# Kernel optimization log

Hardware: AMD Instinct MI355X
Metric: run time of the kernel (lower is better)

Reference implementation:

```python
import jax, jax.numpy as jnp
import numpy as np

B, N, D_IN, D_EMB = 8, 2048, 768, 768

def setup_inputs() -> dict:
    key = jax.random.key(0)
    k1, k2, k3, k4 = jax.random.split(key, 4)
    x = jax.random.normal(k1, (B, N, D_IN), dtype=jnp.float32)
    # nn.Linear weights stored as [out, in]; applied as x @ W.T
    Wq = jax.random.normal(k2, (D_EMB, D_IN), dtype=jnp.float32) * (D_IN ** -0.5)
    Wk = jax.random.normal(k3, (D_EMB, D_IN), dtype=jnp.float32) * (D_IN ** -0.5)
    Wv = jax.random.normal(k4, (D_EMB, D_IN), dtype=jnp.float32) * (D_IN ** -0.5)
    return {"x": x, "Wq": Wq, "Wk": Wk, "Wv": Wv}

def reference(x, Wq, Wk, Wv):
    dim_sqrt = jnp.asarray(D_EMB ** 0.5, x.dtype)
    q = jnp.einsum('bnd,ed->bne', x, Wq)  # [B,N,E]
    k = jnp.einsum('bnd,ed->bne', x, Wk)
    v = jnp.einsum('bnd,ed->bne', x, Wv)
    scores = jnp.einsum('bne,bme->bnm', q, k)  # [B,N,N]
    # NOTE: module applies softmax FIRST, then divides by sqrt(d) (post-hoc)
    attn = jax.nn.softmax(scores, axis=-1) / dim_sqrt
    out = jnp.einsum('bnm,bme->bne', attn, v)
    return out
```

## Files before the change

kernel.cpp:

```cpp
#include <hip/hip_runtime.h>
#include <stdint.h>
#include <type_traits>

typedef __bf16 bf16;
typedef _Float16 f16;
typedef bf16 bf16x8 __attribute__((ext_vector_type(8)));
typedef f16 f16x8 __attribute__((ext_vector_type(8)));
typedef float f32x4 __attribute__((ext_vector_type(4)));

#define LOG2E 1.4426950408889634f
#define SQRT_E 27.712812921102035f

enum { EPI_F32 = 0, EPI_PAIR = 1, EPI_VT = 2, EPI_F16 = 3 };

__device__ __forceinline__ void async16(const void* g, void* l) {
  __builtin_amdgcn_global_load_lds(
      (__attribute__((address_space(1))) void*)(uintptr_t)g,
      (__attribute__((address_space(3))) void*)l, 16, 0, 0);
}

__device__ __forceinline__ f32x4 mfma8(bf16x8 a, bf16x8 b, f32x4 c) {
  return __builtin_amdgcn_mfma_f32_16x16x32_bf16(a, b, c, 0, 0, 0);
}
__device__ __forceinline__ f32x4 mfma8(f16x8 a, f16x8 b, f32x4 c) {
  return __builtin_amdgcn_mfma_f32_16x16x32_f16(a, b, c, 0, 0, 0);
}

template <int N>
__device__ __forceinline__ void vwait() {
  asm volatile("s_waitcnt vmcnt(%0)" ::"i"(N) : "memory");
}
__device__ __forceinline__ void block_bar() {
  asm volatile("" ::: "memory");
  __builtin_amdgcn_s_barrier();
  asm volatile("" ::: "memory");
}

template <typename T, typename TO, int BMt, int BNt, int BKt, int AT, int EPI>
__global__ __launch_bounds__((BMt == 256 ? 512 : 256), 2)
void gemm_pipe(const T* __restrict__ Ah, const T* __restrict__ Al,
               const T* __restrict__ Bh, void* __restrict__ C0,
               int K, long lda, long ldb, long ldc,
               long stA, long stB, long stC, int gxN, int gyM) {
  using vec8 = typename std::conditional<std::is_same<T, bf16>::value,
                                         bf16x8, f16x8>::type;
  static_assert(BMt == BNt, "square tiles only");
  constexpr int THREADS = (BMt == 256) ? 512 : 256;
  constexpr int NWN = (BMt == 256) ? 4 : 2;
  constexpr int WTM = BMt / 2;
  constexpr int WTN = BNt / NWN;
  static_assert(WTN == 64, "wave tile must be 64 wide");
  constexpr int MF = WTM / 16;
  constexpr int KK = BKt / 32;
  constexpr int CPR = BKt / 8;
  constexpr int RPI = THREADS / CPR;
  constexpr int LPP = (BMt * BKt) / (THREADS * 8);
  constexpr int LPT = LPP * (AT == 2 ? 3 : 2);

  __shared__ __align__(16) T sA[2][BMt * BKt];
  __shared__ __align__(16) T sB[2][BNt * BKt];
  __shared__ __align__(16) T sAl[AT == 2 ? 2 * BMt * BKt : 8];

  const int id = blockIdx.x;
  const int xcd = id & 7;
  const int j0 = id >> 3;
  const int s = j0 / gxN;
  const int bxi = j0 - s * gxN;
  const int g = xcd + 8 * s;
  const int byi = g % gyM;
  const int z = g / gyM;

  const T* pA = Ah + (long)z * stA;
  const T* pB = Bh + (long)z * stB;
  const T* pAl = (AT == 2) ? Al : nullptr;

  const int bm = byi * BMt;
  const int bn = bxi * BNt;
  const int tid = threadIdx.x;
  const int wave = tid >> 6;
  const int lane = tid & 63;
  const int wm = (wave / NWN) * WTM;
  const int wn = (wave % NWN) * WTN;
  const int quad = lane >> 4;
  const int l16 = lane & 15;

  f32x4 acc[MF][4] = {};

  const int srow = tid / CPR;
  const int schk = tid % CPR;
  const int swc = ((BKt == 64) ? (schk ^ (srow & 7)) : schk) * 8;
  const int cs0 = (quad * 8) ^ ((BKt == 64) ? ((l16 & 7) << 3) : 0);

  const int NT = K / BKt;

  auto stage = [&](int buf, int t) {
    const long ka = (long)t * BKt + swc;
#pragma unroll
    for (int l = 0; l < LPP; ++l)
      async16(pA + (long)(bm + l * RPI + srow) * lda + ka,
              &sA[buf][(l * THREADS + tid) * 8]);
#pragma unroll
    for (int l = 0; l < LPP; ++l)
      async16(pB + (long)(bn + l * RPI + srow) * ldb + ka,
              &sB[buf][(l * THREADS + tid) * 8]);
    if constexpr (AT == 2) {
#pragma unroll
      for (int l = 0; l < LPP; ++l)
        async16(pAl + (long)(bm + l * RPI + srow) * lda + ka,
                &sAl[buf * BMt * BKt + (l * THREADS + tid) * 8]);
    }
  };

  auto compute = [&](int buf) {
    const T* bA = &sA[buf][0];
    const T* bB = &sB[buf][0];
    const T* bAl = (AT == 2) ? &sAl[buf * BMt * BKt] : nullptr;
    vec8 bf[KK][4];
#pragma unroll
    for (int kk = 0; kk < KK; ++kk)
#pragma unroll
      for (int jj = 0; jj < 4; ++jj)
        bf[kk][jj] =
            *(const vec8*)&bB[(wn + jj * 16 + l16) * BKt + (cs0 ^ (kk * 32))];
#pragma unroll
    for (int mq = 0; mq < MF / 2; ++mq) {
      vec8 af[KK][2];
      vec8 alf[AT == 2 ? KK : 1][2];
#pragma unroll
      for (int kk = 0; kk < KK; ++kk)
#pragma unroll
        for (int ii = 0; ii < 2; ++ii) {
          const int r = wm + mq * 32 + ii * 16 + l16;
          af[kk][ii] = *(const vec8*)&bA[r * BKt + (cs0 ^ (kk * 32))];
          if constexpr (AT == 2)
            alf[kk][ii] = *(const vec8*)&bAl[r * BKt + (cs0 ^ (kk * 32))];
        }
      __builtin_amdgcn_s_setprio(1);
#pragma unroll
      for (int jj = 0; jj < 4; ++jj)
#pragma unroll
        for (int ii = 0; ii < 2; ++ii)
#pragma unroll
          for (int kk = 0; kk < KK; ++kk) {
            acc[mq * 2 + ii][jj] =
                mfma8(af[kk][ii], bf[kk][jj], acc[mq * 2 + ii][jj]);
            if constexpr (AT == 2)
              acc[mq * 2 + ii][jj] =
                  mfma8(alf[kk][ii], bf[kk][jj], acc[mq * 2 + ii][jj]);
          }
      __builtin_amdgcn_s_setprio(0);
    }
  };

  stage(0, 0);
  stage(1, 1);
  vwait<LPT>();
  block_bar();

  for (int t = 0; t < NT; ++t) {
    const int cur = t & 1;
    compute(cur);
    if (t + 1 < NT) {
      block_bar();
      if (t + 2 < NT) {
        stage(cur, t + 2);
        vwait<LPT>();
      } else {
        vwait<0>();
      }
      block_bar();
    }
  }

  if constexpr (EPI == EPI_F32) {
    float* C = (float*)C0 + (long)z * stC;
#pragma unroll
    for (int i = 0; i < MF; ++i) {
      const int mb = bm + wm + i * 16 + quad * 4;
#pragma unroll
      for (int j = 0; j < 4; ++j) {
        const int n = bn + wn + j * 16 + l16;
#pragma unroll
        for (int r = 0; r < 4; ++r)
          C[(long)(mb + r) * ldc + n] = acc[i][j][r];
      }
    }
  } else if constexpr (EPI == EPI_F16) {
    TO* Ch = (TO*)C0;
#pragma unroll
    for (int i = 0; i < MF; ++i) {
      const int mb = bm + wm + i * 16 + quad * 4;
#pragma unroll
      for (int j = 0; j < 4; ++j) {
        const int n = bn + wn + j * 16 + l16;
#pragma unroll
        for (int r = 0; r < 4; ++r)
          Ch[(long)(mb + r) * ldc + n] = (TO)acc[i][j][r];
      }
    }
  } else {
    TO* vT = (TO*)C0;
#pragma unroll
    for (int i = 0; i < MF; ++i) {
      const int mb = bm + wm + i * 16 + quad * 4;
      const long bb = mb >> 11;
      const long ml = mb & 2047;
#pragma unroll
      for (int j = 0; j < 4; ++j) {
        const int e = bn + wn + j * 16 + l16;
        union { TO b[4]; uint2 u; } P;
#pragma unroll
        for (int r = 0; r < 4; ++r) P.b[r] = (TO)acc[i][j][r];
        *(uint2*)&vT[(bb * 768 + e) * 2048 + ml] = P.u;
      }
    }
  }
}

constexpr int BM = 128, BN = 128, BK = 64;

template <typename T, typename TO, int AT, int BT, int EPI, int SWZ>
__global__ __launch_bounds__(256)
void gemm_kernel(const T* __restrict__ Ah, const T* __restrict__ Al,
                 const T* __restrict__ Bh, const T* __restrict__ Bl,
                 void* __restrict__ C0, void* __restrict__ C1,
                 int K, long lda, long ldb, long ldbl, long ldc,
                 long stA, long stB, long stBl, long stC,
                 int gxN, int gyM) {
  using vec8 = typename std::conditional<std::is_same<T, bf16>::value,
                                         bf16x8, f16x8>::type;
  __shared__ __align__(16) T sAh[BM * BK];
  __shared__ __align__(16) T sBh[BN * BK];
  __shared__ __align__(16) T sAl[AT == 2 ? BM * BK : 8];
  __shared__ __align__(16) T sBl[BT == 2 ? BN * BK : 8];

  int bxi, byi, z;
  if constexpr (SWZ) {
    const int id = blockIdx.x;
    const int xcd = id & 7;
    const int j = id >> 3;
    const int s = j / gxN;
    const int n = j - s * gxN;
    const int g = xcd + 8 * s;
    bxi = n;
    byi = g % gyM;
    z = g / gyM;
  } else {
    bxi = blockIdx.x; byi = blockIdx.y; z = blockIdx.z;
  }

  const T* pAh = Ah + (long)z * stA;
  const T* pBh = Bh + (long)z * stB;
  const T* pAl = (AT == 2) ? (Al + (long)z * stA) : nullptr;
  const T* pBl = (BT == 2) ? (Bl + (long)z * stBl) : nullptr;

  const int bm = byi * BM;
  const int bn = bxi * BN;
  const int tid = threadIdx.x;
  const int wave = tid >> 6;
  const int lane = tid & 63;
  const int wm = (wave & 1) * 64;
  const int wn = (wave >> 1) * 64;
  const int quad = lane >> 4;
  const int l16 = lane & 15;

  f32x4 acc[4][4] = {};

  const int sr0 = tid >> 3;
  const int swc = ((tid & 7) ^ (sr0 & 7)) * 8;
  const int cs0 = (quad * 8) ^ ((l16 & 7) << 3);

  for (int kt = 0; kt < K; kt += BK) {
    __syncthreads();
    {
      const long ka = kt + swc;
#pragma unroll
      for (int l = 0; l < 4; ++l) {
        const int row = l * 32 + sr0;
        async16(pAh + (long)(bm + row) * lda + ka, &sAh[(l * 256 + tid) * 8]);
      }
#pragma unroll
      for (int l = 0; l < 4; ++l) {
        const int row = l * 32 + sr0;
        async16(pBh + (long)(bn + row) * ldb + ka, &sBh[(l * 256 + tid) * 8]);
      }
      if constexpr (AT == 2) {
#pragma unroll
        for (int l = 0; l < 4; ++l) {
          const int row = l * 32 + sr0;
          async16(pAl + (long)(bm + row) * lda + ka, &sAl[(l * 256 + tid) * 8]);
        }
      }
      if constexpr (BT == 2) {
#pragma unroll
        for (int l = 0; l < 4; ++l) {
          const int row = l * 32 + sr0;
          async16(pBl + (long)(bn + row) * ldbl + ka, &sBl[(l * 256 + tid) * 8]);
        }
      }
    }
    __syncthreads();

#pragma unroll
    for (int kk = 0; kk < 2; ++kk) {
      const int cs = cs0 ^ (kk * 32);
      vec8 ah[4], al[4];
#pragma unroll
      for (int i = 0; i < 4; ++i) {
        ah[i] = *(const vec8*)&sAh[(wm + i * 16 + l16) * BK + cs];
        if constexpr (AT == 2)
          al[i] = *(const vec8*)&sAl[(wm + i * 16 + l16) * BK + cs];
      }
#pragma unroll
      for (int j = 0; j < 4; ++j) {
        const vec8 bh = *(const vec8*)&sBh[(wn + j * 16 + l16) * BK + cs];
        vec8 bl;
        if constexpr (BT == 2)
          bl = *(const vec8*)&sBl[(wn + j * 16 + l16) * BK + cs];
#pragma unroll
        for (int i = 0; i < 4; ++i) {
          acc[i][j] = mfma8(ah[i], bh, acc[i][j]);
          if constexpr (BT == 2) acc[i][j] = mfma8(ah[i], bl, acc[i][j]);
          if constexpr (AT == 2) acc[i][j] = mfma8(al[i], bh, acc[i][j]);
        }
      }
    }
  }

  if constexpr (EPI == EPI_PAIR) {
    TO* Ch = (TO*)C0;
    TO* Cl = (TO*)C1;
#pragma unroll
    for (int i = 0; i < 4; ++i) {
      const int mb = bm + wm + i * 16 + quad * 4;
#pragma unroll
      for (int j = 0; j < 4; ++j) {
        const int n = bn + wn + j * 16 + l16;
#pragma unroll
        for (int r = 0; r < 4; ++r) {
          const float f = acc[i][j][r];
          const TO h = (TO)f;
          const long idx = (long)(mb + r) * ldc + n;
          Ch[idx] = h;
          Cl[idx] = (TO)(f - (float)h);
        }
      }
    }
  }
}

__global__ __launch_bounds__(256)
void softmax_kernel(float* __restrict__ sc) {
  __shared__ float red[4];
  float* srow = sc + (long)blockIdx.x * 2048;
  const int tid = threadIdx.x;
  const int wave = tid >> 6;
  const int lane = tid & 63;
  const float4 v0 = *(const float4*)(srow + tid * 4);
  const float4 v1 = *(const float4*)(srow + 1024 + tid * 4);
  float mx = fmaxf(fmaxf(fmaxf(v0.x, v0.y), fmaxf(v0.z, v0.w)),
                   fmaxf(fmaxf(v1.x, v1.y), fmaxf(v1.z, v1.w)));
#pragma unroll
  for (int o = 32; o >= 1; o >>= 1) mx = fmaxf(mx, __shfl_xor(mx, o));
  if (lane == 0) red[wave] = mx;
  __syncthreads();
  mx = fmaxf(fmaxf(red[0], red[1]), fmaxf(red[2], red[3]));
  const float e0 = exp2f((v0.x - mx) * LOG2E);
  const float e1 = exp2f((v0.y - mx) * LOG2E);
  const float e2 = exp2f((v0.z - mx) * LOG2E);
  const float e3 = exp2f((v0.w - mx) * LOG2E);
  const float e4 = exp2f((v1.x - mx) * LOG2E);
  const float e5 = exp2f((v1.y - mx) * LOG2E);
  const float e6 = exp2f((v1.z - mx) * LOG2E);
  const float e7 = exp2f((v1.w - mx) * LOG2E);
  float s = ((e0 + e1) + (e2 + e3)) + ((e4 + e5) + (e6 + e7));
#pragma unroll
  for (int o = 32; o >= 1; o >>= 1) s += __shfl_xor(s, o);
  __syncthreads();
  if (lane == 0) red[wave] = s;
  __syncthreads();
  s = red[0] + red[1] + red[2] + red[3];
  const float inv = 1.0f / (s * SQRT_E);
  f16* prow = (f16*)srow;
  union { f16 b[4]; uint2 u; } P;
  P.b[0] = (f16)(e0 * inv); P.b[1] = (f16)(e1 * inv);
  P.b[2] = (f16)(e2 * inv); P.b[3] = (f16)(e3 * inv);
  *(uint2*)(prow + tid * 4) = P.u;
  P.b[0] = (f16)(e4 * inv); P.b[1] = (f16)(e5 * inv);
  P.b[2] = (f16)(e6 * inv); P.b[3] = (f16)(e7 * inv);
  *(uint2*)(prow + 1024 + tid * 4) = P.u;
}

__global__ __launch_bounds__(256)
void split_all(const float4* __restrict__ x, const float4* __restrict__ wv,
               uint2* __restrict__ xh, uint2* __restrict__ xl,
               uint2* __restrict__ wvh) {
  constexpr int NX = 3145728;
  constexpr int NWV = 147456;
  const int i = blockIdx.x * 256 + threadIdx.x;
  float4 v;
  uint2 *dh, *dl;
  if (i < NX) {
    v = x[i]; dh = xh + i; dl = xl + i;
  } else {
    const int m = i - NX;
    if (m >= NWV) return;
    v = wv[m]; dh = wvh + m; dl = nullptr;
  }
  const f16 h0 = (f16)v.x, h1 = (f16)v.y, h2 = (f16)v.z, h3 = (f16)v.w;
  union { f16 b[4]; uint2 u; } P;
  P.b[0] = h0; P.b[1] = h1; P.b[2] = h2; P.b[3] = h3;
  *dh = P.u;
  if (dl != nullptr) {
    P.b[0] = (f16)(v.x - (float)h0);
    P.b[1] = (f16)(v.y - (float)h1);
    P.b[2] = (f16)(v.z - (float)h2);
    P.b[3] = (f16)(v.w - (float)h3);
    *dl = P.u;
  }
}

__global__ __launch_bounds__(256)
void transpose_split(const float* __restrict__ Wq, const float* __restrict__ Wk,
                     f16* __restrict__ qTh, f16* __restrict__ qTl,
                     f16* __restrict__ kTh, f16* __restrict__ kTl) {
  __shared__ float tile[64][65];
  const float* src = blockIdx.z ? Wk : Wq;
  f16* dh = blockIdx.z ? kTh : qTh;
  f16* dl = blockIdx.z ? kTl : qTl;
  const int e0 = blockIdx.y * 64, d0 = blockIdx.x * 64;
  const int t = threadIdx.x;
  const int r = t >> 2;
  const int c4 = (t & 3) * 16;
  const float4* s4 = (const float4*)(src + (long)(e0 + r) * 768 + d0 + c4);
#pragma unroll
  for (int g = 0; g < 4; ++g) {
    const float4 v = s4[g];
    tile[r][c4 + g * 4 + 0] = v.x;
    tile[r][c4 + g * 4 + 1] = v.y;
    tile[r][c4 + g * 4 + 2] = v.z;
    tile[r][c4 + g * 4 + 3] = v.w;
  }
  __syncthreads();
  union { f16 b[8]; uint4 u; } H0, H1, L0, L1;
#pragma unroll
  for (int i = 0; i < 16; ++i) {
    const float v = tile[c4 + i][r];
    const f16 h = (f16)v;
    const f16 l = (f16)(v - (float)h);
    if (i < 8) { H0.b[i] = h; L0.b[i] = l; }
    else       { H1.b[i - 8] = h; L1.b[i - 8] = l; }
  }
  const long o = (long)(d0 + r) * 768 + e0 + c4;
  *(uint4*)(dh + o) = H0.u;  *(uint4*)(dh + o + 8) = H1.u;
  *(uint4*)(dl + o) = L0.u;  *(uint4*)(dl + o + 8) = L1.u;
}

extern "C" void kernel_launch(void* const* d_in, const int* in_sizes, int n_in,
                              void* d_out, int out_size, void* d_ws, size_t ws_size,
                              hipStream_t stream) {
  const float* x  = (const float*)d_in[0];
  const float* Wq = (const float*)d_in[1];
  const float* Wk = (const float*)d_in[2];
  const float* Wv = (const float*)d_in[3];
  float* out = (float*)d_out;
  char* ws = (char*)d_ws;

  const size_t SZ = 25165824;
  f16* yh = (f16*)(ws + 0 * SZ);
  f16* xh = (f16*)(ws + 2 * SZ);
  f16* vT = (f16*)(ws + 3 * SZ);
  const size_t PERS = 4 * SZ;
  const size_t WT = 1179648;
  f16* xl   = (f16*)(ws + PERS);
  f16* wqTh = (f16*)(ws + PERS + SZ);
  f16* wqTl = (f16*)(ws + PERS + SZ + 1 * WT);
  f16* wkTh = (f16*)(ws + PERS + SZ + 2 * WT);
  f16* wkTl = (f16*)(ws + PERS + SZ + 3 * WT);
  f16* mtH  = (f16*)(ws + PERS + SZ + 4 * WT);
  f16* mtL  = (f16*)(ws + PERS + SZ + 5 * WT);
  f16* wvh  = (f16*)(ws + PERS + SZ + 6 * WT);
  float* scores = (float*)(ws + PERS);

  long avail = (long)ws_size - (long)PERS;
  int nb = (int)(avail / 16777216);
  if (nb < 1) nb = 1;
  if (nb > 8) nb = 8;

  split_all<<<12864, 256, 0, stream>>>(
      (const float4*)x, (const float4*)Wv, (uint2*)xh, (uint2*)xl, (uint2*)wvh);
  transpose_split<<<dim3(12, 12, 2), 256, 0, stream>>>(
      Wq, Wk, wqTh, wqTl, wkTh, wkTl);

  gemm_kernel<f16, f16, 2, 2, EPI_PAIR, 0><<<dim3(6, 6, 1), 256, 0, stream>>>(
      wkTh, wkTl, wqTh, wqTl, (void*)mtH, (void*)mtL,
      768, 768, 768, 768, 768, 0, 0, 0, 0, 0, 0);

  gemm_pipe<f16, f16, 128, 128, 32, 2, EPI_F16><<<768, 256, 0, stream>>>(
      xh, xl, mtH, (void*)yh, 768, 768, 768, 768, 0, 0, 0, 6, 128);

  gemm_pipe<f16, f16, 128, 128, 64, 1, EPI_VT><<<768, 256, 0, stream>>>(
      xh, nullptr, wvh, (void*)vT, 768, 768, 768, 0, 0, 0, 0, 6, 128);

  const long RS = 1572864;
  const long VTS = 1572864;
  for (int b0 = 0; b0 < 8; b0 += nb) {
    const int nbg = (8 - b0 < nb) ? (8 - b0) : nb;
    gemm_pipe<f16, float, 256, 256, 64, 1, EPI_F32><<<64 * nbg, 512, 0, stream>>>(
        yh + (long)b0 * RS, nullptr, xh + (long)b0 * RS, (void*)scores,
        768, 768, 768, 2048, RS, RS, 4194304L, 8, 8);
    softmax_kernel<<<nbg * 2048, 256, 0, stream>>>(scores);
    gemm_pipe<f16, float, 128, 128, 64, 1, EPI_F32><<<96 * nbg, 256, 0, stream>>>(
        (const f16*)scores, nullptr, vT + (long)b0 * VTS,
        (void*)(out + (long)b0 * 1572864),
        2048, 4096, 2048, 768, 8388608L, VTS, 1572864L, 6, 16);
  }
}
```

Before: 376.6 us.

## Add triple-buffered ring GEMM with split-phase staging for scores and PV

Adds a new 256x256-tile GEMM kernel using a three-stage LDS ring with BK=32. Each iteration splits into two half-tile MFMA phases, interleaving async global-to-LDS loads for iteration t+2 with compute, and raises wave priority around the MFMA blocks. It also remaps blocks to XCDs by batch index. The QK^T scores GEMM and the attention-times-V GEMM now use this kernel, and the PV GEMM moves from 128x128 to 256x256 tiles with fewer blocks. In exchange it uses more LDS and more barriers per K-step, and the PV launch now has fewer blocks to fill the GPU.

```diff
diff --git a/kernel.cpp b/kernel.cpp
--- a/kernel.cpp
+++ b/kernel.cpp
@@ -34,6 +34,187 @@
   asm volatile("" ::: "memory");
   __builtin_amdgcn_s_barrier();
   asm volatile("" ::: "memory");
+}
+__device__ __forceinline__ void lgkm0() {
+  asm volatile("s_waitcnt lgkmcnt(0)" ::: "memory");
+}
+__device__ __forceinline__ void spin() { __builtin_amdgcn_sched_barrier(0); }
+
+template <typename T, typename TO, int AT, int EPI>
+__global__ __launch_bounds__(512, 2)
+void gemm_ring(const T* __restrict__ Ah, const T* __restrict__ Al,
+               const T* __restrict__ Bh, void* __restrict__ C0,
+               int K, long lda, long ldb, long ldc,
+               long stA, long stB, long stC, int gxN, int gyM, int nz) {
+  using vec8 = typename std::conditional<std::is_same<T, bf16>::value,
+                                         bf16x8, f16x8>::type;
+  constexpr int LPT = (AT == 2) ? 6 : 4;
+  __shared__ __align__(16) T sA[3][256 * 32];
+  __shared__ __align__(16) T sB[3][256 * 32];
+  __shared__ __align__(16) T sAl[AT == 2 ? 3 * 256 * 32 : 8];
+
+  const int id = blockIdx.x;
+  const int xcd = id & 7;
+  const int j0 = id >> 3;
+  const int s = j0 / gxN;
+  const int bxi = j0 - s * gxN;
+  const int g = xcd + 8 * s;
+  int byi, z;
+  if (nz > 0) { z = g % nz; byi = g / nz; }
+  else        { byi = g % gyM; z = g / gyM; }
+
+  const T* pA = Ah + (long)z * stA;
+  const T* pB = Bh + (long)z * stB;
+  const T* pAl = (AT == 2) ? Al : nullptr;
+
+  const int bm = byi * 256;
+  const int bn = bxi * 256;
+  const int tid = threadIdx.x;
+  const int wave = tid >> 6;
+  const int lane = tid & 63;
+  const int wm = (wave >> 2) * 128;
+  const int wn = (wave & 3) * 64;
+  const int quad = lane >> 4;
+  const int l16 = lane & 15;
+
+  f32x4 acc[8][4] = {};
+
+  const int srow = tid >> 2;
+  const int swc = ((tid & 3) ^ ((tid >> 3) & 3)) * 8;
+  const int cread = (quad ^ ((l16 >> 1) & 3)) * 8;
+
+  const int NT = K / 32;
+
+  auto stageA = [&](int buf, int t, int l) {
+    const long ka = (long)t * 32 + swc;
+    async16(pA + (long)(bm + l * 128 + srow) * lda + ka,
+            &sA[buf][(l * 512 + tid) * 8]);
+  };
+  auto stageB = [&](int buf, int t, int l) {
+    const long ka = (long)t * 32 + swc;
+    async16(pB + (long)(bn + l * 128 + srow) * ldb + ka,
+            &sB[buf][(l * 512 + tid) * 8]);
+  };
+  auto stageAl = [&](int buf, int t, int l) {
+    const long ka = (long)t * 32 + swc;
+    async16(pAl + (long)(bm + l * 128 + srow) * lda + ka,
+            &sAl[buf * 8192 + (l * 512 + tid) * 8]);
+  };
+
+  stageA(0, 0, 0); stageA(0, 0, 1); stageB(0, 0, 0); stageB(0, 0, 1);
+  if constexpr (AT == 2) { stageAl(0, 0, 0); stageAl(0, 0, 1); }
+  stageA(1, 1, 0); stageA(1, 1, 1); stageB(1, 1, 0); stageB(1, 1, 1);
+  if constexpr (AT == 2) { stageAl(1, 1, 0); stageAl(1, 1, 1); }
+  vwait<LPT>();
+  block_bar();
+
+  int cur = 0, b2 = 2;
+  for (int t = 0; t < NT; ++t) {
+    const bool st = (t + 2 < NT);
+    vec8 bfr[4], af[4], alf[AT == 2 ? 4 : 1];
+#pragma unroll
+    for (int j = 0; j < 4; ++j)
+      bfr[j] = *(const vec8*)&sB[cur][(wn + j * 16 + l16) * 32 + cread];
+#pragma unroll
+    for (int i = 0; i < 4; ++i) {
+      af[i] = *(const vec8*)&sA[cur][(wm + i * 16 + l16) * 32 + cread];
+      if constexpr (AT == 2)
+        alf[i] = *(const vec8*)&sAl[cur * 8192 + (wm + i * 16 + l16) * 32 + cread];
+    }
+    if (st) {
+      stageA(b2, t + 2, 0); stageA(b2, t + 2, 1);
+      if constexpr (AT == 2) stageAl(b2, t + 2, 0);
+    }
+    block_bar();
+    lgkm0();
+    spin();
+    __builtin_amdgcn_s_setprio(1);
+#pragma unroll
+    for (int j = 0; j < 4; ++j)
+#pragma unroll
+      for (int i = 0; i < 4; ++i) {
+        acc[i][j] = mfma8(af[i], bfr[j], acc[i][j]);
+        if constexpr (AT == 2) acc[i][j] = mfma8(alf[i], bfr[j], acc[i][j]);
+      }
+    __builtin_amdgcn_s_setprio(0);
+    spin();
+    block_bar();
+    vec8 af2[4], alf2[AT == 2 ? 4 : 1];
+#pragma unroll
+    for (int i = 0; i < 4; ++i) {
+      af2[i] = *(const vec8*)&sA[cur][(wm + 64 + i * 16 + l16) * 32 + cread];
+      if constexpr (AT == 2)
+        alf2[i] =
+            *(const vec8*)&sAl[cur * 8192 + (wm + 64 + i * 16 + l16) * 32 + cread];
+    }
+    if (st) {
+      stageB(b2, t + 2, 0); stageB(b2, t + 2, 1);
+      if constexpr (AT == 2) stageAl(b2, t + 2, 1);
+    }
+    block_bar();
+    lgkm0();
+    spin();
+    __builtin_amdgcn_s_setprio(1);
+#pragma unroll
+    for (int j = 0; j < 4; ++j)
+#pragma unroll
+      for (int i = 0; i < 4; ++i) {
+        acc[4 + i][j] = mfma8(af2[i], bfr[j], acc[4 + i][j]);
+        if constexpr (AT == 2) acc[4 + i][j] = mfma8(alf2[i], bfr[j], acc[4 + i][j]);
+      }
+    __builtin_amdgcn_s_setprio(0);
+    spin();
+    if (t + 1 < NT) {
+      if (st) vwait<LPT>(); else vwait<0>();
+      block_bar();
+    }
+    cur = (cur == 2) ? 0 : cur + 1;
+    b2 = (b2 == 2) ? 0 : b2 + 1;
+  }
+
+  if constexpr (EPI == EPI_F32) {
+    float* C = (float*)C0 + (long)z * stC;
+#pragma unroll
+    for (int i = 0; i < 8; ++i) {
+      const int mb = bm + wm + i * 16 + quad * 4;
+#pragma unroll
+      for (int j = 0; j < 4; ++j) {
+        const int n = bn + wn + j * 16 + l16;
+#pragma unroll
+        for (int r = 0; r < 4; ++r)
+          C[(long)(mb + r) * ldc + n] = acc[i][j][r];
+      }
+    }
+  } else if constexpr (EPI == EPI_F16) {
+    TO* Ch = (TO*)C0;
+#pragma unroll
+    for (int i = 0; i < 8; ++i) {
+      const int mb = bm + wm + i * 16 + quad * 4;
+#pragma unroll
+      for (int j = 0; j < 4; ++j) {
+        const int n = bn + wn + j * 16 + l16;
+#pragma unroll
+        for (int r = 0; r < 4; ++r)
+          Ch[(long)(mb + r) * ldc + n] = (TO)acc[i][j][r];
+      }
+    }
+  } else {
+    TO* vT = (TO*)C0;
+#pragma unroll
+    for (int i = 0; i < 8; ++i) {
+      const int mb = bm + wm + i * 16 + quad * 4;
+      const long bb = mb >> 11;
+      const long ml = mb & 2047;
+#pragma unroll
+      for (int j = 0; j < 4; ++j) {
+        const int e = bn + wn + j * 16 + l16;
+        union { TO b[4]; uint2 u; } P;
+#pragma unroll
+        for (int r = 0; r < 4; ++r) P.b[r] = (TO)acc[i][j][r];
+        *(uint2*)&vT[(bb * 768 + e) * 2048 + ml] = P.u;
+      }
+    }
+  }
 }
 
 template <typename T, typename TO, int BMt, int BNt, int BKt, int AT, int EPI>
@@ -172,8 +353,8 @@
     }
   }
 
-  if constexpr (EPI == EPI_F32) {
-    float* C = (float*)C0 + (long)z * stC;
+  if constexpr (EPI == EPI_F16) {
+    TO* Ch = (TO*)C0;
 #pragma unroll
     for (int i = 0; i < MF; ++i) {
       const int mb = bm + wm + i * 16 + quad * 4;
@@ -182,23 +363,10 @@
         const int n = bn + wn + j * 16 + l16;
 #pragma unroll
         for (int r = 0; r < 4; ++r)
-          C[(long)(mb + r) * ldc + n] = acc[i][j][r];
-      }
-    }
-  } else if constexpr (EPI == EPI_F16) {
-    TO* Ch = (TO*)C0;
-#pragma unroll
-    for (int i = 0; i < MF; ++i) {
-      const int mb = bm + wm + i * 16 + quad * 4;
-#pragma unroll
-      for (int j = 0; j < 4; ++j) {
-        const int n = bn + wn + j * 16 + l16;
-#pragma unroll
-        for (int r = 0; r < 4; ++r)
           Ch[(long)(mb + r) * ldc + n] = (TO)acc[i][j][r];
       }
     }
-  } else {
+  } else if constexpr (EPI == EPI_VT) {
     TO* vT = (TO*)C0;
 #pragma unroll
     for (int i = 0; i < MF; ++i) {
@@ -212,6 +380,19 @@
 #pragma unroll
         for (int r = 0; r < 4; ++r) P.b[r] = (TO)acc[i][j][r];
         *(uint2*)&vT[(bb * 768 + e) * 2048 + ml] = P.u;
+      }
+    }
+  } else {
+    float* C = (float*)C0 + (long)z * stC;
+#pragma unroll
+    for (int i = 0; i < MF; ++i) {
+      const int mb = bm + wm + i * 16 + quad * 4;
+#pragma unroll
+      for (int j = 0; j < 4; ++j) {
+        const int n = bn + wn + j * 16 + l16;
+#pragma unroll
+        for (int r = 0; r < 4; ++r)
+          C[(long)(mb + r) * ldc + n] = acc[i][j][r];
       }
     }
   }
@@ -506,13 +687,13 @@
   const long VTS = 1572864;
   for (int b0 = 0; b0 < 8; b0 += nb) {
     const int nbg = (8 - b0 < nb) ? (8 - b0) : nb;
-    gemm_pipe<f16, float, 256, 256, 64, 1, EPI_F32><<<64 * nbg, 512, 0, stream>>>(
+    gemm_ring<f16, float, 1, EPI_F32><<<64 * nbg, 512, 0, stream>>>(
         yh + (long)b0 * RS, nullptr, xh + (long)b0 * RS, (void*)scores,
-        768, 768, 768, 2048, RS, RS, 4194304L, 8, 8);
+        768, 768, 768, 2048, RS, RS, 4194304L, 8, 8, nbg);
     softmax_kernel<<<nbg * 2048, 256, 0, stream>>>(scores);
-    gemm_pipe<f16, float, 128, 128, 64, 1, EPI_F32><<<96 * nbg, 256, 0, stream>>>(
+    gemm_ring<f16, float, 1, EPI_F32><<<24 * nbg, 512, 0, stream>>>(
         (const f16*)scores, nullptr, vT + (long)b0 * VTS,
         (void*)(out + (long)b0 * 1572864),
-        2048, 4096, 2048, 768, 8388608L, VTS, 1572864L, 6, 16);
-  }
-}
+        2048, 4096, 2048, 768, 8388608L, VTS, 1572864L, 3, 8, nbg);
+  }
+}
```

Result: faster. 366.1 us (-2.8%).
